# Kernel optimization log

Measured on AMD Instinct MI355X. Metric: run time of the kernel, lower is better.

The kernel has to match this reference:

```python
import jax, jax.numpy as jnp
import numpy as np

B, S, D = 4, 2048, 1024  # batch, seq_len, d_emb (even for Givens pairs)


def givens_rotate(r, x):
    """Apply 2x2 Givens block rotations defined by r [D] to x [..., D]."""
    g = r.reshape(-1, 2)
    g = g / jnp.linalg.norm(g, axis=-1, keepdims=True)  # normalize (cos, sin) pairs
    xp = x.reshape(x.shape[:-1] + (x.shape[-1] // 2, 2))
    c, s = g[:, 0], g[:, 1]
    y0 = c * xp[..., 0] - s * xp[..., 1]
    y1 = c * xp[..., 1] + s * xp[..., 0]
    return jnp.stack([y0, y1], axis=-1).reshape(x.shape)


def setup_inputs() -> dict:
    key = jax.random.key(0)
    k1, k2 = jax.random.split(key, 2)
    Q = jax.random.normal(k1, (B, S, D), dtype=jnp.float32)
    # QKV_rotation.weight ~ U(-1, 1) per original init (before the identity overwrite)
    rot_w = jax.random.uniform(k2, (3, D), dtype=jnp.float32, minval=-1.0, maxval=1.0)
    scale = jnp.array([np.sqrt(D)], dtype=jnp.float32)
    bias = jnp.zeros((), dtype=jnp.float32)
    return {"Q": Q, "rot_w": rot_w, "scale": scale, "bias": bias}


def reference(Q, rot_w, scale, bias):
    # Givens-rotation 'projections' for q/k/v
    q = givens_rotate(rot_w[0], Q)
    k = givens_rotate(rot_w[1], Q)
    v = givens_rotate(rot_w[2], Q)
    # prepend zero time coordinate -> points on the Lorentz model ambient space
    zeros = jnp.zeros(Q.shape[:-1] + (1,), Q.dtype)
    q = jnp.concatenate([zeros, q], axis=-1)[:, None]  # [B,1,S,D+1]
    k = jnp.concatenate([zeros, k], axis=-1)[:, None]
    v = jnp.concatenate([zeros, v], axis=-1)[:, None]
    # Lorentz signature (-, +, +, ...)
    sgn = jnp.concatenate([-jnp.ones((1,), Q.dtype), jnp.ones((q.shape[-1] - 1,), Q.dtype)])
    # cinner(q, k): time-negated inner product -> scores [B,1,S,S]
    cin = jnp.einsum('bhqd,bhkd->bhqk', q * sgn, k)
    attn = jax.nn.softmax((2.0 + 2.0 * cin) / scale + bias, axis=-1)
    # Lorentz mid-point: weighted sum normalized by sqrt(|<m,m>_L|)
    ave = jnp.einsum('bhqk,bhkd->bhqd', attn, v)
    inner = jnp.sum(ave * ave * sgn, axis=-1, keepdims=True)
    denom = jnp.sqrt(jnp.clip(jnp.abs(inner), 1e-8, None))
    out = (ave / denom)[:, 0]  # [B,S,D+1]
    return out[..., 1:]  # drop time coordinate -> [B,S,D]
```

## Files before the change

### kernel.cpp

```cpp
#include <hip/hip_runtime.h>

typedef _Float16 h16;
typedef _Float16 half8 __attribute__((ext_vector_type(8)));
typedef _Float16 half4v __attribute__((ext_vector_type(4)));
typedef float floatx4 __attribute__((ext_vector_type(4)));

static constexpr int Bb_ = 4, S_ = 2048, D_ = 1024;

static __device__ __forceinline__ void gl_lds16(const void* g, void* l) {
  __builtin_amdgcn_global_load_lds(
      (const __attribute__((address_space(1))) unsigned int*)g,
      (__attribute__((address_space(3))) unsigned int*)l, 16, 0, 0);
}

__global__ __launch_bounds__(256) void k_prep_t(const float* __restrict__ Q,
                                                const float* __restrict__ rot,
                                                h16* __restrict__ Qh,
                                                h16* __restrict__ Kh,
                                                h16* __restrict__ VhT) {
  __shared__ __align__(16) h16 tile[64][64];
  int d0 = blockIdx.x * 64, s0 = blockIdx.y * 64, b = blockIdx.z;
  int t = threadIdx.x;
  const float* Qb = Q + ((size_t)b * S_ + s0) * D_ + d0;
  h16* Qhb = Qh + ((size_t)b * S_ + s0) * D_ + d0;
  h16* Khb = Kh + ((size_t)b * S_ + s0) * D_ + d0;
#pragma unroll
  for (int i = 0; i < 4; ++i) {
    int c = t + 256 * i;
    int row = c >> 4;
    int col = (c & 15) * 4;
    float4 q = *(const float4*)&Qb[(size_t)row * D_ + col];
    int dg = (d0 + col) >> 2;
    float4 r0 = ((const float4*)rot)[dg];
    float4 r1 = ((const float4*)rot)[D_ / 4 + dg];
    float4 r2 = ((const float4*)rot)[2 * D_ / 4 + dg];
    float inq0 = rsqrtf(r0.x * r0.x + r0.y * r0.y);
    float ink0 = rsqrtf(r1.x * r1.x + r1.y * r1.y);
    float cc0 = (r0.x * r1.x + r0.y * r1.y) * inq0 * ink0;
    float ss0 = (r0.x * r1.y - r0.y * r1.x) * inq0 * ink0;
    float y0 = cc0 * q.x - ss0 * q.y;
    float y1 = cc0 * q.y + ss0 * q.x;
    float inq1 = rsqrtf(r0.z * r0.z + r0.w * r0.w);
    float ink1 = rsqrtf(r1.z * r1.z + r1.w * r1.w);
    float cc1 = (r0.z * r1.z + r0.w * r1.w) * inq1 * ink1;
    float ss1 = (r0.z * r1.w - r0.w * r1.z) * inq1 * ink1;
    float y2 = cc1 * q.z - ss1 * q.w;
    float y3 = cc1 * q.w + ss1 * q.z;
    float inv0 = rsqrtf(r2.x * r2.x + r2.y * r2.y);
    float cv0 = r2.x * inv0, sv0 = r2.y * inv0;
    float v0 = cv0 * q.x - sv0 * q.y;
    float v1 = cv0 * q.y + sv0 * q.x;
    float inv1 = rsqrtf(r2.z * r2.z + r2.w * r2.w);
    float cv1 = r2.z * inv1, sv1 = r2.w * inv1;
    float v2 = cv1 * q.z - sv1 * q.w;
    float v3 = cv1 * q.w + sv1 * q.z;
    half4v kh = {(h16)y0, (h16)y1, (h16)y2, (h16)y3};
    half4v qh = {(h16)q.x, (h16)q.y, (h16)q.z, (h16)q.w};
    half4v vh = {(h16)v0, (h16)v1, (h16)v2, (h16)v3};
    *(half4v*)&Qhb[(size_t)row * D_ + col] = qh;
    *(half4v*)&Khb[(size_t)row * D_ + col] = kh;
    int pcol = col ^ ((row >> 3) << 3);
    *(half4v*)&tile[row][pcol] = vh;
  }
  __syncthreads();
  h16* dst = VhT + ((size_t)b * D_ + d0) * S_ + s0;
#pragma unroll
  for (int i = 0; i < 2; ++i) {
    int c = t + 256 * i;
    int drow = c >> 3;
    int sc = (c & 7) * 8;
    int xr = sc;
    half8 v;
#pragma unroll
    for (int j = 0; j < 8; ++j) v[j] = tile[sc + j][drow ^ xr];
    *(half8*)&dst[(size_t)drow * S_ + sc] = v;
  }
}

#define G_FENCE asm volatile("" ::: "memory")
#define G_BAR                     \
  do {                            \
    G_FENCE;                      \
    __builtin_amdgcn_s_barrier(); \
    G_FENCE;                      \
  } while (0)

template <int NF, bool OUT16>
__global__ __launch_bounds__(512) void k_gemm8(
    const char* __restrict__ A, int a_pitch, unsigned long long a_batch,
    const char* __restrict__ Bt, int b_pitch, unsigned long long b_batch,
    void* __restrict__ C, int c_pitch, unsigned long long c_batch, int Kdim) {
  constexpr int BNR = NF * 64;
  constexpr int JQ = NF / 2;
  __shared__ __align__(16) h16 As[2][2][256 * 32];
  __shared__ __align__(16) h16 Bs[2][2][BNR * 32];
  const int t = threadIdx.x;
  const int lane = t & 63;
  const int w = t >> 6;
  const int wm = (w >> 2) * 128;
  const int wn = (w & 3) * (NF * 16);
  const int id = blockIdx.x + 8 * (blockIdx.y + 8 * blockIdx.z);
  const int L = (id & 7) * 32 + (id >> 3);
  const int tm = L & 7, tn = (L >> 3) & 7, tz = L >> 6;
  const char* Ab = A + (unsigned long long)tz * a_batch +
                   (unsigned long long)(tm * 256) * (unsigned long long)a_pitch;
  const char* Bb = Bt + (unsigned long long)tz * b_batch +
                   (unsigned long long)(tn * BNR) * (unsigned long long)b_pitch;
  const int srow = t >> 2;
  const int scol = ((t & 3) ^ ((t >> 3) & 3)) << 4;
  const int lds_o = t * 16;
  const int mrow = lane & 15, kc = lane >> 4;
  const int koff = (kc ^ ((mrow >> 1) & 3)) << 3;
  const int NT = Kdim >> 6;

#define SG_A(bf, kt, hm)                                                      \
  do {                                                                        \
    const char* sp_ = Ab +                                                    \
                      (unsigned long long)(srow + (hm) * 128) * a_pitch +     \
                      (kt) * 128 + scol;                                      \
    gl_lds16(sp_, (char*)&As[bf][0][(hm) * 128 * 32] + lds_o);                \
    gl_lds16(sp_ + 64, (char*)&As[bf][1][(hm) * 128 * 32] + lds_o);           \
  } while (0)
#define SG_B(bf, kt, hm)                                                      \
  do {                                                                        \
    const char* sp_ = Bb +                                                    \
                      (unsigned long long)(srow + (hm) * 128) * b_pitch +     \
                      (kt) * 128 + scol;                                      \
    gl_lds16(sp_, (char*)&Bs[bf][0][(hm) * 128 * 32] + lds_o);                \
    gl_lds16(sp_ + 64, (char*)&Bs[bf][1][(hm) * 128 * 32] + lds_o);           \
  } while (0)

  half8 a[4][2], b[2][JQ][2];
  floatx4 acc[8][NF];
#pragma unroll
  for (int i = 0; i < 8; ++i)
#pragma unroll
    for (int j = 0; j < NF; ++j) acc[i][j] = (floatx4){0.f, 0.f, 0.f, 0.f};

#define LDA_(bf, mh)                                                           \
  do {                                                                         \
    _Pragma("unroll") for (int i_ = 0; i_ < 4; ++i_) {                         \
      a[i_][0] = *(const half8*)&As[bf][0]                                     \
                     [(wm + ((mh) * 4 + i_) * 16 + mrow) * 32 + koff];         \
      a[i_][1] = *(const half8*)&As[bf][1]                                     \
                     [(wm + ((mh) * 4 + i_) * 16 + mrow) * 32 + koff];         \
    }                                                                          \
  } while (0)
#define LDB_(bf, nh)                                                           \
  do {                                                                         \
    _Pragma("unroll") for (int j_ = 0; j_ < JQ; ++j_) {                        \
      b[nh][j_][0] = *(const half8*)&Bs[bf][0]                                 \
                         [(wn + ((nh) * JQ + j_) * 16 + mrow) * 32 + koff];    \
      b[nh][j_][1] = *(const half8*)&Bs[bf][1]                                 \
                         [(wn + ((nh) * JQ + j_) * 16 + mrow) * 32 + koff];    \
    }                                                                          \
  } while (0)
#define QUAD(mh, nh)                                                           \
  do {                                                                         \
    __builtin_amdgcn_s_setprio(1);                                             \
    _Pragma("unroll") for (int i_ = 0; i_ < 4; ++i_)                           \
        _Pragma("unroll") for (int j_ = 0; j_ < JQ; ++j_) {                    \
      acc[(mh) * 4 + i_][(nh) * JQ + j_] =                                     \
          __builtin_amdgcn_mfma_f32_16x16x32_f16(                              \
              a[i_][0], b[nh][j_][0], acc[(mh) * 4 + i_][(nh) * JQ + j_], 0,   \
              0, 0);                                                           \
      acc[(mh) * 4 + i_][(nh) * JQ + j_] =                                     \
          __builtin_amdgcn_mfma_f32_16x16x32_f16(                              \
              a[i_][1], b[nh][j_][1], acc[(mh) * 4 + i_][(nh) * JQ + j_], 0,   \
              0, 0);                                                           \
    }                                                                          \
    __builtin_amdgcn_s_setprio(0);                                             \
  } while (0)

  SG_A(0, 0, 0);
  SG_A(0, 0, 1);
  SG_B(0, 0, 0);
  if constexpr (NF == 4) SG_B(0, 0, 1);
  SG_B(1, 1, 0);
  if constexpr (NF == 4) SG_B(1, 1, 1);
  SG_A(1, 1, 0);
  if constexpr (NF == 4)
    asm volatile("s_waitcnt vmcnt(6)" ::: "memory");
  else
    asm volatile("s_waitcnt vmcnt(4)" ::: "memory");
  G_BAR;

#define TILE_(bf, nb, u)                                                       \
  do {                                                                         \
    const int k1_ = ((u) + 1 < NT) ? (u) + 1 : NT - 1;                         \
    const int k2_ = ((u) + 2 < NT) ? (u) + 2 : NT - 1;                         \
                                                                       \
    LDA_(bf, 0);                                                               \
    LDB_(bf, 0);                                                               \
    SG_A(nb, k1_, 1);                                                          \
    G_BAR;                                                                     \
    QUAD(0, 0);                                                                \
    G_BAR;                                                                     \
                                                                       \
    LDB_(bf, 1);                                                               \
    G_BAR;                                                                     \
    QUAD(0, 1);                                                                \
    G_BAR;                                                                     \
                                                                       \
    LDA_(bf, 1);                                                               \
    SG_B(bf, k2_, 0);                                                          \
    G_BAR;                                                                     \
    QUAD(1, 0);                                                                \
    G_BAR;                                                                     \
                                                                       \
    if constexpr (NF == 4) SG_B(bf, k2_, 1);                                   \
    SG_A(bf, k2_, 0);                                                          \
    if constexpr (NF == 4)                                                     \
      asm volatile("s_waitcnt vmcnt(6)" ::: "memory");                         \
    else                                                                       \
      asm volatile("s_waitcnt vmcnt(4)" ::: "memory");                         \
    G_BAR;                                                                     \
    QUAD(1, 1);                                                                \
    G_BAR;                                                                     \
  } while (0)

  for (int u = 0; u < NT; u += 2) {
    TILE_(0, 1, u);
    TILE_(1, 0, u + 1);
  }
  asm volatile("s_waitcnt vmcnt(0)" ::: "memory");

  const int m0 = tm * 256 + wm;
  const int n0 = tn * BNR + wn;
  const int ccol = lane & 15;
  const int rq = (lane >> 4) * 4;
  if constexpr (OUT16) {
    h16* Cb = (h16*)C + (unsigned long long)tz * c_batch;
#pragma unroll
    for (int i = 0; i < 8; ++i)
#pragma unroll
      for (int j = 0; j < NF; ++j)
#pragma unroll
        for (int r = 0; r < 4; ++r)
          Cb[(unsigned long long)(m0 + i * 16 + rq + r) * c_pitch +
             (n0 + j * 16 + ccol)] = (h16)acc[i][j][r];
  } else {
    float* Cb = (float*)C + (unsigned long long)tz * c_batch;
#pragma unroll
    for (int i = 0; i < 8; ++i)
#pragma unroll
      for (int j = 0; j < NF; ++j)
#pragma unroll
        for (int r = 0; r < 4; ++r)
          Cb[(unsigned long long)(m0 + i * 16 + rq + r) * c_pitch +
             (n0 + j * 16 + ccol)] = acc[i][j][r];
  }
#undef TILE_
#undef QUAD
#undef LDB_
#undef LDA_
#undef SG_B
#undef SG_A
}

__global__ __launch_bounds__(256) void k_softmax(h16* __restrict__ Sl,
                                                 const float* __restrict__ scale_p) {
  int wv = threadIdx.x >> 6, ln = threadIdx.x & 63;
  int row = blockIdx.x * 4 + wv;
  h16* base = Sl + (size_t)row * S_;
  half8 c[4];
#pragma unroll
  for (int r = 0; r < 4; ++r) c[r] = ((const half8*)base)[ln + 64 * r];
  float m = -1e30f;
#pragma unroll
  for (int r = 0; r < 4; ++r)
#pragma unroll
    for (int j = 0; j < 8; ++j) m = fmaxf(m, (float)c[r][j]);
#pragma unroll
  for (int off = 32; off; off >>= 1) m = fmaxf(m, __shfl_xor(m, off));
  float alpha = 2.0f / scale_p[0];
#pragma unroll
  for (int r = 0; r < 4; ++r) {
    half8 pv;
#pragma unroll
    for (int j = 0; j < 8; ++j) pv[j] = (h16)__expf(((float)c[r][j] - m) * alpha);
    ((half8*)base)[ln + 64 * r] = pv;
  }
}

__global__ __launch_bounds__(256) void k_epilogue(float* __restrict__ O) {
  int wv = threadIdx.x >> 6, ln = threadIdx.x & 63;
  int row = blockIdx.x * 4 + wv;
  float* base = O + (size_t)row * D_;
  float4 u[4];
#pragma unroll
  for (int r = 0; r < 4; ++r) u[r] = ((const float4*)base)[ln + 64 * r];
  float ss = 0.f;
#pragma unroll
  for (int r = 0; r < 4; ++r)
    ss += u[r].x * u[r].x + u[r].y * u[r].y + u[r].z * u[r].z + u[r].w * u[r].w;
#pragma unroll
  for (int off = 32; off; off >>= 1) ss += __shfl_xor(ss, off);
  float f = rsqrtf(fmaxf(ss, 1e-30f));
#pragma unroll
  for (int r = 0; r < 4; ++r) {
    float4 o;
    o.x = u[r].x * f;
    o.y = u[r].y * f;
    o.z = u[r].z * f;
    o.w = u[r].w * f;
    ((float4*)base)[ln + 64 * r] = o;
  }
}

extern "C" void kernel_launch(void* const* d_in, const int* in_sizes, int n_in,
                              void* d_out, int out_size, void* d_ws, size_t ws_size,
                              hipStream_t stream) {
  const float* Q = (const float*)d_in[0];
  const float* rot = (const float*)d_in[1];
  const float* scale = (const float*)d_in[2];
  float* O = (float*)d_out;
  char* ws = (char*)d_ws;
  const size_t MB = 1024ull * 1024ull;
  h16* Qh = (h16*)(ws);
  h16* Kh = (h16*)(ws + 16 * MB);
  h16* VhT = (h16*)(ws + 32 * MB);
  h16* Sl = (h16*)(ws + 48 * MB);

  k_prep_t<<<dim3(D_ / 64, S_ / 64, Bb_), 256, 0, stream>>>(Q, rot, Qh, Kh, VhT);
  k_gemm8<4, true><<<dim3(8, 8, 4), 512, 0, stream>>>(
      (const char*)Qh, D_ * 2, (unsigned long long)S_ * D_ * 2,
      (const char*)Kh, D_ * 2, (unsigned long long)S_ * D_ * 2,
      (void*)Sl, S_, (unsigned long long)S_ * S_, D_);
  k_softmax<<<dim3(Bb_ * S_ / 4), 256, 0, stream>>>(Sl, scale);
  k_gemm8<2, false><<<dim3(8, 8, 4), 512, 0, stream>>>(
      (const char*)Sl, S_ * 2, (unsigned long long)S_ * S_ * 2,
      (const char*)VhT, S_ * 2, (unsigned long long)D_ * S_ * 2,
      (void*)O, D_, (unsigned long long)S_ * D_, S_);
  k_epilogue<<<dim3(Bb_ * S_ / 4), 256, 0, stream>>>(O);
}
```

Before: 194.2 us.

## Double-buffer MFMA register fragments to overlap LDS reads with matrix math

The GEMM kernel now keeps two register sets for the A and B fragments. It issues LDS reads for the next quadrant, including the first quadrant of the next K tile, before running the MFMAs for the current one, and drops several barriers between quadrants. It also sets launch_bounds to (512, 2) to ask for two blocks per CU. The aim is to hide LDS latency behind MFMA work and cut barrier stalls, at the cost of higher register pressure and a tighter register budget, which could cause spills. Removing barriers also makes the ordering between async global-to-LDS writes and LDS reads more delicate.

After: 194.0 us. Within noise of the previous version (-0.1%).

```diff
diff --git a/kernel.cpp b/kernel.cpp
--- a/kernel.cpp
+++ b/kernel.cpp
@@ -86,7 +86,7 @@
   } while (0)
 
 template <int NF, bool OUT16>
-__global__ __launch_bounds__(512) void k_gemm8(
+__global__ __launch_bounds__(512, 2) void k_gemm8(
     const char* __restrict__ A, int a_pitch, unsigned long long a_batch,
     const char* __restrict__ Bt, int b_pitch, unsigned long long b_batch,
     void* __restrict__ C, int c_pitch, unsigned long long c_batch, int Kdim) {
@@ -113,63 +113,63 @@
   const int koff = (kc ^ ((mrow >> 1) & 3)) << 3;
   const int NT = Kdim >> 6;
 
-#define SG_A(bf, kt, hm)                                                      \
-  do {                                                                        \
-    const char* sp_ = Ab +                                                    \
-                      (unsigned long long)(srow + (hm) * 128) * a_pitch +     \
-                      (kt) * 128 + scol;                                      \
-    gl_lds16(sp_, (char*)&As[bf][0][(hm) * 128 * 32] + lds_o);                \
-    gl_lds16(sp_ + 64, (char*)&As[bf][1][(hm) * 128 * 32] + lds_o);           \
-  } while (0)
-#define SG_B(bf, kt, hm)                                                      \
-  do {                                                                        \
-    const char* sp_ = Bb +                                                    \
-                      (unsigned long long)(srow + (hm) * 128) * b_pitch +     \
-                      (kt) * 128 + scol;                                      \
-    gl_lds16(sp_, (char*)&Bs[bf][0][(hm) * 128 * 32] + lds_o);                \
-    gl_lds16(sp_ + 64, (char*)&Bs[bf][1][(hm) * 128 * 32] + lds_o);           \
-  } while (0)
-
-  half8 a[4][2], b[2][JQ][2];
+#define SG_A(bf, kt, hm)                                                  \
+  do {                                                                    \
+    const char* sp_ = Ab +                                                \
+                      (unsigned long long)(srow + (hm) * 128) * a_pitch + \
+                      (kt) * 128 + scol;                                  \
+    gl_lds16(sp_, (char*)&As[bf][0][(hm) * 128 * 32] + lds_o);            \
+    gl_lds16(sp_ + 64, (char*)&As[bf][1][(hm) * 128 * 32] + lds_o);       \
+  } while (0)
+#define SG_B(bf, kt, hm)                                                  \
+  do {                                                                    \
+    const char* sp_ = Bb +                                                \
+                      (unsigned long long)(srow + (hm) * 128) * b_pitch + \
+                      (kt) * 128 + scol;                                  \
+    gl_lds16(sp_, (char*)&Bs[bf][0][(hm) * 128 * 32] + lds_o);            \
+    gl_lds16(sp_ + 64, (char*)&Bs[bf][1][(hm) * 128 * 32] + lds_o);       \
+  } while (0)
+
+  half8 ar0[4][2], ar1[4][2], br0[JQ][2], br1[JQ][2];
   floatx4 acc[8][NF];
 #pragma unroll
   for (int i = 0; i < 8; ++i)
 #pragma unroll
     for (int j = 0; j < NF; ++j) acc[i][j] = (floatx4){0.f, 0.f, 0.f, 0.f};
 
-#define LDA_(bf, mh)                                                           \
-  do {                                                                         \
-    _Pragma("unroll") for (int i_ = 0; i_ < 4; ++i_) {                         \
-      a[i_][0] = *(const half8*)&As[bf][0]                                     \
-                     [(wm + ((mh) * 4 + i_) * 16 + mrow) * 32 + koff];         \
-      a[i_][1] = *(const half8*)&As[bf][1]                                     \
-                     [(wm + ((mh) * 4 + i_) * 16 + mrow) * 32 + koff];         \
-    }                                                                          \
-  } while (0)
-#define LDB_(bf, nh)                                                           \
-  do {                                                                         \
-    _Pragma("unroll") for (int j_ = 0; j_ < JQ; ++j_) {                        \
-      b[nh][j_][0] = *(const half8*)&Bs[bf][0]                                 \
-                         [(wn + ((nh) * JQ + j_) * 16 + mrow) * 32 + koff];    \
-      b[nh][j_][1] = *(const half8*)&Bs[bf][1]                                 \
-                         [(wn + ((nh) * JQ + j_) * 16 + mrow) * 32 + koff];    \
-    }                                                                          \
-  } while (0)
-#define QUAD(mh, nh)                                                           \
-  do {                                                                         \
-    __builtin_amdgcn_s_setprio(1);                                             \
-    _Pragma("unroll") for (int i_ = 0; i_ < 4; ++i_)                           \
-        _Pragma("unroll") for (int j_ = 0; j_ < JQ; ++j_) {                    \
-      acc[(mh) * 4 + i_][(nh) * JQ + j_] =                                     \
-          __builtin_amdgcn_mfma_f32_16x16x32_f16(                              \
-              a[i_][0], b[nh][j_][0], acc[(mh) * 4 + i_][(nh) * JQ + j_], 0,   \
-              0, 0);                                                           \
-      acc[(mh) * 4 + i_][(nh) * JQ + j_] =                                     \
-          __builtin_amdgcn_mfma_f32_16x16x32_f16(                              \
-              a[i_][1], b[nh][j_][1], acc[(mh) * 4 + i_][(nh) * JQ + j_], 0,   \
-              0, 0);                                                           \
-    }                                                                          \
-    __builtin_amdgcn_s_setprio(0);                                             \
+#define LDA_(bf, mh, DST)                                              \
+  do {                                                                 \
+    _Pragma("unroll") for (int i_ = 0; i_ < 4; ++i_) {                 \
+      DST[i_][0] = *(const half8*)&As[bf][0]                           \
+                       [(wm + ((mh) * 4 + i_) * 16 + mrow) * 32 + koff]; \
+      DST[i_][1] = *(const half8*)&As[bf][1]                           \
+                       [(wm + ((mh) * 4 + i_) * 16 + mrow) * 32 + koff]; \
+    }                                                                  \
+  } while (0)
+#define LDB_(bf, nh, DST)                                              \
+  do {                                                                 \
+    _Pragma("unroll") for (int j_ = 0; j_ < JQ; ++j_) {                \
+      DST[j_][0] = *(const half8*)&Bs[bf][0]                           \
+                       [(wn + ((nh)*JQ + j_) * 16 + mrow) * 32 + koff]; \
+      DST[j_][1] = *(const half8*)&Bs[bf][1]                           \
+                       [(wn + ((nh)*JQ + j_) * 16 + mrow) * 32 + koff]; \
+    }                                                                  \
+  } while (0)
+#define QUAD(mh, nh, AF, BF)                                                 \
+  do {                                                                       \
+    __builtin_amdgcn_s_setprio(1);                                           \
+    _Pragma("unroll") for (int i_ = 0; i_ < 4; ++i_)                         \
+        _Pragma("unroll") for (int j_ = 0; j_ < JQ; ++j_) {                  \
+      acc[(mh) * 4 + i_][(nh)*JQ + j_] =                                     \
+          __builtin_amdgcn_mfma_f32_16x16x32_f16(                            \
+              AF[i_][0], BF[j_][0], acc[(mh) * 4 + i_][(nh)*JQ + j_], 0, 0,  \
+              0);                                                            \
+      acc[(mh) * 4 + i_][(nh)*JQ + j_] =                                     \
+          __builtin_amdgcn_mfma_f32_16x16x32_f16(                            \
+              AF[i_][1], BF[j_][1], acc[(mh) * 4 + i_][(nh)*JQ + j_], 0, 0,  \
+              0);                                                            \
+    }                                                                        \
+    __builtin_amdgcn_s_setprio(0);                                           \
   } while (0)
 
   SG_A(0, 0, 0);
@@ -184,39 +184,37 @@
   else
     asm volatile("s_waitcnt vmcnt(4)" ::: "memory");
   G_BAR;
-
-#define TILE_(bf, nb, u)                                                       \
-  do {                                                                         \
-    const int k1_ = ((u) + 1 < NT) ? (u) + 1 : NT - 1;                         \
-    const int k2_ = ((u) + 2 < NT) ? (u) + 2 : NT - 1;                         \
-                                                                       \
-    LDA_(bf, 0);                                                               \
-    LDB_(bf, 0);                                                               \
-    SG_A(nb, k1_, 1);                                                          \
-    G_BAR;                                                                     \
-    QUAD(0, 0);                                                                \
-    G_BAR;                                                                     \
-                                                                       \
-    LDB_(bf, 1);                                                               \
-    G_BAR;                                                                     \
-    QUAD(0, 1);                                                                \
-    G_BAR;                                                                     \
-                                                                       \
-    LDA_(bf, 1);                                                               \
-    SG_B(bf, k2_, 0);                                                          \
-    G_BAR;                                                                     \
-    QUAD(1, 0);                                                                \
-    G_BAR;                                                                     \
-                                                                       \
-    if constexpr (NF == 4) SG_B(bf, k2_, 1);                                   \
-    SG_A(bf, k2_, 0);                                                          \
-    if constexpr (NF == 4)                                                     \
-      asm volatile("s_waitcnt vmcnt(6)" ::: "memory");                         \
-    else                                                                       \
-      asm volatile("s_waitcnt vmcnt(4)" ::: "memory");                         \
-    G_BAR;                                                                     \
-    QUAD(1, 1);                                                                \
-    G_BAR;                                                                     \
+  LDA_(0, 0, ar0);
+  LDB_(0, 0, br0);
+
+#define TILE_(bf, nb, u)                                     \
+  do {                                                       \
+    const int k1_ = ((u) + 1 < NT) ? (u) + 1 : NT - 1;       \
+    const int k2_ = ((u) + 2 < NT) ? (u) + 2 : NT - 1;       \
+                                                     \
+    SG_A(nb, k1_, 1);                                        \
+    G_BAR;                                                   \
+    LDB_(bf, 1, br1);                                        \
+    QUAD(0, 0, ar0, br0);                                    \
+                                                     \
+    G_BAR;                                                   \
+    LDA_(bf, 1, ar1);                                        \
+    QUAD(0, 1, ar0, br1);                                    \
+                                                     \
+    SG_B(bf, k2_, 0);                                        \
+    G_BAR;                                                   \
+    QUAD(1, 0, ar1, br0);                                    \
+                                                     \
+    if constexpr (NF == 4) SG_B(bf, k2_, 1);                 \
+    SG_A(bf, k2_, 0);                                        \
+    if constexpr (NF == 4)                                   \
+      asm volatile("s_waitcnt vmcnt(6)" ::: "memory");       \
+    else                                                     \
+      asm volatile("s_waitcnt vmcnt(4)" ::: "memory");       \
+    G_BAR;                                                   \
+    LDA_(nb, 0, ar0);    \
+    LDB_(nb, 0, br0);                                        \
+    QUAD(1, 1, ar1, br1);                                    \
   } while (0)
 
   for (int u = 0; u < NT; u += 2) {
```
